# Performance work log

Hardware: AMD Instinct MI355X
Metric: run time of the kernel (lower is better)

Reference implementation:

```python
import jax, jax.numpy as jnp
import numpy as np

N_NODES = 100000
N_EDGES = 1600000
N_GRAPHS = 512


def gcn_conv(x, row, col, W, b):
    # x: [N, Cin], row/col: [E] (self-loops already appended)
    n = x.shape[0]
    h = x @ W                                        # [N, Cout]
    deg = jax.ops.segment_sum(jnp.ones_like(col, dtype=x.dtype), col, num_segments=n)
    dinv = jnp.where(deg > 0, deg ** -0.5, 0.0)
    norm = dinv[row] * dinv[col]                     # [E]
    msg = norm[:, None] * h[row]                     # [E, Cout]
    out = jax.ops.segment_sum(msg, col, num_segments=n)
    return out + b


def setup_inputs() -> dict:
    key = jax.random.key(0)
    ks = jax.random.split(key, 10)
    x = jax.random.normal(ks[0], (N_NODES, 128), dtype=jnp.float32)
    edge_index = jax.random.randint(ks[1], (2, N_EDGES), 0, N_NODES, dtype=jnp.int64)
    batch = jnp.sort(jax.random.randint(ks[2], (N_NODES,), 0, N_GRAPHS, dtype=jnp.int64))
    def lin_w(k, fan_in, fan_out):
        bound = 1.0 / np.sqrt(fan_in)
        return jax.random.uniform(k, (fan_in, fan_out), jnp.float32, -bound, bound)
    # GCN layers (bias zero-initialized per reset_parameters)
    W1 = lin_w(ks[3], 128, 128); b1 = jnp.zeros((128,), jnp.float32)
    W2 = lin_w(ks[4], 128, 128); b2 = jnp.zeros((128,), jnp.float32)
    # MLP layers (Linear with bias)
    Wm1 = lin_w(ks[5], 128, 64)
    bm1 = jax.random.uniform(ks[6], (64,), jnp.float32, -1/np.sqrt(128), 1/np.sqrt(128))
    Wm2 = lin_w(ks[7], 64, 1)
    bm2 = jax.random.uniform(ks[8], (1,), jnp.float32, -1/np.sqrt(64), 1/np.sqrt(64))
    return {"x": x, "edge_index": edge_index, "batch": batch,
            "W1": W1, "b1": b1, "W2": W2, "b2": b2,
            "Wm1": Wm1, "bm1": bm1, "Wm2": Wm2, "bm2": bm2}


def reference(x, edge_index, batch, W1, b1, W2, b2, Wm1, bm1, Wm2, bm2):
    n = x.shape[0]
    loops = jnp.arange(n, dtype=edge_index.dtype)
    row = jnp.concatenate([edge_index[0], loops])
    col = jnp.concatenate([edge_index[1], loops])
    # GCN: conv -> relu -> conv
    h = gcn_conv(x, row, col, W1, b1)
    h = jax.nn.relu(h)
    h = gcn_conv(h, row, col, W2, b2)
    # scatter-mean pooling over graphs
    sums = jax.ops.segment_sum(h, batch, num_segments=N_GRAPHS)      # [G, C]
    counts = jax.ops.segment_sum(jnp.ones((n,), h.dtype), batch, num_segments=N_GRAPHS)
    g = sums / jnp.maximum(counts, 1.0)[:, None]
    # MLP: linear -> relu -> linear
    g = jax.nn.relu(g @ Wm1 + bm1)
    out = g @ Wm2 + bm2
    return out
```

## Files before the change

kernel.cpp:

```cpp
#include <hip/hip_runtime.h>
#include <math.h>

#define C_DIM 128
#define POOL_CHUNK 64
#define BKT_SHIFT 7
#define MAX_B 1024
#define CB 256
typedef unsigned short ushort_t;
typedef __attribute__((ext_vector_type(8))) short short8;
typedef __attribute__((ext_vector_type(4))) float f32x4;

static inline int ceil_div(int a, int b) { return (a + b - 1) / b; }

__device__ inline ushort_t f2bf(float f) {
    union { float f; unsigned u; } v; v.f = f;
    unsigned r = v.u + 0x7FFFu + ((v.u >> 16) & 1u);
    return (ushort_t)(r >> 16);
}
__device__ inline float bf2f(unsigned s) {
    union { unsigned u; float f; } v; v.u = s << 16; return v.f;
}
__device__ inline float bf_lo(unsigned u) {
    union { unsigned v; float f; } c; c.v = u << 16; return c.f;
}
__device__ inline float bf_hi(unsigned u) {
    union { unsigned v; float f; } c; c.v = u & 0xFFFF0000u; return c.f;
}
__device__ inline void accum8(uint4 u, float acc[8]) {
    acc[0] += bf_lo(u.x); acc[1] += bf_hi(u.x);
    acc[2] += bf_lo(u.y); acc[3] += bf_hi(u.y);
    acc[4] += bf_lo(u.z); acc[5] += bf_hi(u.z);
    acc[6] += bf_lo(u.w); acc[7] += bf_hi(u.w);
}


__global__ __launch_bounds__(256) void k_bcount(
    const int* __restrict__ col, int E, int chunk, int B,
    int* __restrict__ counts) {
    __shared__ int hist[MAX_B];
    int t = threadIdx.x;
    for (int i = t; i < B; i += 256) hist[i] = 0;
    __syncthreads();
    int s = blockIdx.x * chunk;
    int e = s + chunk; if (e > E) e = E;
    for (int i = s + 4 * t; i < e; i += 1024) {
        int4 c = *(const int4*)(col + i);
        atomicAdd(&hist[c.x >> BKT_SHIFT], 1);
        atomicAdd(&hist[c.y >> BKT_SHIFT], 1);
        atomicAdd(&hist[c.z >> BKT_SHIFT], 1);
        atomicAdd(&hist[c.w >> BKT_SHIFT], 1);
    }
    __syncthreads();
    for (int i = t; i < B; i += 256)
        counts[(size_t)i * CB + blockIdx.x] = hist[i];
}

__global__ __launch_bounds__(256) void k_bscan(
    int* __restrict__ counts, int* __restrict__ btot) {
    __shared__ int sd[256];
    int b = blockIdx.x, t = threadIdx.x;
    int v = counts[(size_t)b * CB + t];
    sd[t] = v;
    __syncthreads();
    for (int off = 1; off < 256; off <<= 1) {
        int x = (t >= off) ? sd[t - off] : 0;
        __syncthreads();
        sd[t] += x;
        __syncthreads();
    }
    counts[(size_t)b * CB + t] = sd[t] - v;
    if (t == 255) btot[b] = sd[255];
}

__global__ __launch_bounds__(256) void k_btotscan(
    const int* __restrict__ btot, int* __restrict__ bbase, int B, int E,
    int* __restrict__ offs, int N) {
    __shared__ int sd[256];
    __shared__ int carry_s;
    int t = threadIdx.x;
    if (t == 0) carry_s = 0;
    __syncthreads();
    int nc = (B + 255) / 256;
    for (int c = 0; c < nc; ++c) {
        int idx = c * 256 + t;
        int v = (idx < B) ? btot[idx] : 0;
        sd[t] = v;
        __syncthreads();
        for (int off = 1; off < 256; off <<= 1) {
            int x = (t >= off) ? sd[t - off] : 0;
            __syncthreads();
            sd[t] += x;
            __syncthreads();
        }
        int pre = sd[t] - v + carry_s;
        if (idx < B) bbase[idx] = pre;
        __syncthreads();
        if (t == 0) carry_s += sd[255];
        __syncthreads();
    }
    if (t == 0) { bbase[B] = E; offs[N] = E; }
}

__global__ __launch_bounds__(256) void k_bscatter(
    const int* __restrict__ row, const int* __restrict__ col, int E, int chunk,
    int B, const int* __restrict__ counts, const int* __restrict__ bbase,
    int2* __restrict__ epk) {
    __shared__ int cur[MAX_B];
    int t = threadIdx.x, blk = blockIdx.x;
    for (int i = t; i < B; i += 256)
        cur[i] = bbase[i] + counts[(size_t)i * CB + blk];
    __syncthreads();
    int s = blk * chunk;
    int e = s + chunk; if (e > E) e = E;
    for (int i = s + 4 * t; i < e; i += 1024) {
        int4 c = *(const int4*)(col + i);
        int4 r = *(const int4*)(row + i);
        int s0 = atomicAdd(&cur[c.x >> BKT_SHIFT], 1); epk[s0] = make_int2(r.x, c.x);
        int s1 = atomicAdd(&cur[c.y >> BKT_SHIFT], 1); epk[s1] = make_int2(r.y, c.y);
        int s2 = atomicAdd(&cur[c.z >> BKT_SHIFT], 1); epk[s2] = make_int2(r.z, c.z);
        int s3 = atomicAdd(&cur[c.w >> BKT_SHIFT], 1); epk[s3] = make_int2(r.w, c.w);
    }
}

__global__ __launch_bounds__(256) void k_bfinal(
    const int2* __restrict__ epk, const int* __restrict__ bbase, int N,
    int* __restrict__ offs, float* __restrict__ dinv, int* __restrict__ csr) {
    __shared__ int cnt[128];
    __shared__ int pre[128];
    __shared__ int cur[128];
    int bkt = blockIdx.x, t = threadIdx.x;
    int s = bbase[bkt], e = bbase[bkt + 1];
    int base = bkt << BKT_SHIFT;
    int nn = N - base; if (nn > 128) nn = 128;
    if (t < 128) cnt[t] = 0;
    __syncthreads();
    for (int i = s + t; i < e; i += 256)
        atomicAdd(&cnt[epk[i].y & 127], 1);
    __syncthreads();
    if (t < 128) pre[t] = cnt[t];
    __syncthreads();
    for (int off = 1; off < 128; off <<= 1) {
        int x = (t >= off && t < 128) ? pre[t - off] : 0;
        __syncthreads();
        if (t < 128) pre[t] += x;
        __syncthreads();
    }
    if (t < 128) {
        int ex = pre[t] - cnt[t];
        cur[t] = ex;
        if (t < nn) {
            offs[base + t] = s + ex;
            dinv[base + t] = 1.0f / sqrtf((float)cnt[t] + 1.0f);
        }
    }
    __syncthreads();
    for (int i = s + t; i < e; i += 256) {
        int2 rc = epk[i];
        int slot = atomicAdd(&cur[rc.y & 127], 1);
        csr[s + slot] = rc.x;
    }
}

__global__ __launch_bounds__(256) void k_wfrag(
    const float* __restrict__ W, uint4* __restrict__ wf) {
    int t = threadIdx.x;
    for (int f = t; f < 2048; f += 256) {
        int lane = f & 63, kkn = f >> 6;
        int kk = kkn & 3, nt = kkn >> 2;
        int n = lane & 15, quad = lane >> 4;
        union { ushort_t h[8]; uint4 v; } u;
#pragma unroll
        for (int j = 0; j < 8; ++j)
            u.h[j] = f2bf(W[(size_t)(kk * 32 + quad * 8 + j) * C_DIM + nt * 16 + n]);
        wf[f] = u.v;
    }
}

template <int ABF16>
__global__ __launch_bounds__(256) void k_matmul_mfma(
    const float* __restrict__ Af, const ushort_t* __restrict__ Abf,
    const uint4* __restrict__ wfrag, const float* __restrict__ dinv,
    ushort_t* __restrict__ Cb, int N) {
    __shared__ __align__(16) ushort_t eb[64 * 136];
    int t = threadIdx.x;
    int wv = t >> 6, lane = t & 63;
    int n = lane & 15, quad = lane >> 4;
    int row0 = blockIdx.x * 64;
    int rowA = row0 + wv * 16 + n;
    int rowAc = rowA < N ? rowA : N - 1;

    f32x4 acc[8];
#pragma unroll
    for (int i = 0; i < 8; ++i) acc[i] = (f32x4){0.f, 0.f, 0.f, 0.f};

#pragma unroll
    for (int kk = 0; kk < 4; ++kk) {
        short8 a;
        if (ABF16) {
            uint4 u = *(const uint4*)(Abf + (size_t)rowAc * C_DIM + kk * 32 + quad * 8);
            union { uint4 v; short8 s; } c; c.v = u;
            a = c.s;
        } else {
            const float4* ap = (const float4*)(Af + (size_t)rowAc * C_DIM + kk * 32 + quad * 8);
            float4 f0 = ap[0], f1 = ap[1];
            union { ushort_t h[8]; short8 s; } c;
            c.h[0] = f2bf(f0.x); c.h[1] = f2bf(f0.y); c.h[2] = f2bf(f0.z); c.h[3] = f2bf(f0.w);
            c.h[4] = f2bf(f1.x); c.h[5] = f2bf(f1.y); c.h[6] = f2bf(f1.z); c.h[7] = f2bf(f1.w);
            a = c.s;
        }
#pragma unroll
        for (int nt = 0; nt < 8; ++nt) {
            uint4 bu = wfrag[(nt * 4 + kk) * 64 + lane];
            union { uint4 v; short8 s; } c; c.v = bu;
            acc[nt] = __builtin_amdgcn_mfma_f32_16x16x32_bf16(a, c.s, acc[nt], 0, 0, 0);
        }
    }

#pragma unroll
    for (int reg = 0; reg < 4; ++reg) {
        int rl = wv * 16 + quad * 4 + reg;
        int r = row0 + rl;
        float s = dinv[r < N ? r : N - 1];
#pragma unroll
        for (int nt = 0; nt < 8; ++nt)
            eb[rl * 136 + nt * 16 + n] = f2bf(acc[nt][reg] * s);
    }
    __syncthreads();
    int rows = N - row0; if (rows > 64) rows = 64;
    for (int idx = t; idx < 16 * 64; idx += 256) {
        int r = idx >> 4, c8 = idx & 15;
        if (r < rows)
            *(uint4*)(Cb + (size_t)(row0 + r) * C_DIM + c8 * 8) =
                *(const uint4*)&eb[r * 136 + c8 * 8];
    }
}

template <int RELU>
__global__ __launch_bounds__(256) void k_aggregate(
    const ushort_t* __restrict__ hs, const int* __restrict__ offs,
    const int* __restrict__ csr, const float* __restrict__ dinv,
    const float* __restrict__ bias, uint4* __restrict__ outV, int N) {
    int node = (blockIdx.x << 2) + (threadIdx.x >> 6);
    if (node >= N) return;
    int t = threadIdx.x & 63;
    int q = t >> 4;
    int fs = t & 15;
    int s = offs[node], e = offs[node + 1];

    float acc[8];
    {
        uint4 u = *(const uint4*)(hs + (size_t)node * C_DIM + fs * 8);
        float v[8];
        v[0] = bf_lo(u.x); v[1] = bf_hi(u.x);
        v[2] = bf_lo(u.y); v[3] = bf_hi(u.y);
        v[4] = bf_lo(u.z); v[5] = bf_hi(u.z);
        v[6] = bf_lo(u.w); v[7] = bf_hi(u.w);
#pragma unroll
        for (int i = 0; i < 8; ++i) acc[i] = (q == 0) ? v[i] : 0.f;
    }

    int j = s;
    for (; j + 16 <= e; j += 16) {
        int r[4];
#pragma unroll
        for (int b = 0; b < 4; ++b) r[b] = csr[j + b * 4 + q];
        uint4 u[4];
#pragma unroll
        for (int b = 0; b < 4; ++b)
            u[b] = *(const uint4*)(hs + (size_t)r[b] * C_DIM + fs * 8);
#pragma unroll
        for (int b = 0; b < 4; ++b) accum8(u[b], acc);
    }
    for (; j + 4 <= e; j += 4) {
        int r = csr[j + q];
        uint4 u = *(const uint4*)(hs + (size_t)r * C_DIM + fs * 8);
        accum8(u, acc);
    }
    if (j + q < e) {
        int r = csr[j + q];
        uint4 u = *(const uint4*)(hs + (size_t)r * C_DIM + fs * 8);
        accum8(u, acc);
    }

#pragma unroll
    for (int i = 0; i < 8; ++i) {
        acc[i] += __shfl_xor(acc[i], 16);
        acc[i] += __shfl_xor(acc[i], 32);
    }

    if (q == 0) {
        float dn = dinv[node];
        float4 b0 = *(const float4*)(bias + fs * 8);
        float4 b1 = *(const float4*)(bias + fs * 8 + 4);
        float o[8];
        o[0] = dn * acc[0] + b0.x; o[1] = dn * acc[1] + b0.y;
        o[2] = dn * acc[2] + b0.z; o[3] = dn * acc[3] + b0.w;
        o[4] = dn * acc[4] + b1.x; o[5] = dn * acc[5] + b1.y;
        o[6] = dn * acc[6] + b1.z; o[7] = dn * acc[7] + b1.w;
        if (RELU) {
#pragma unroll
            for (int i = 0; i < 8; ++i) o[i] = fmaxf(o[i], 0.f);
        }
        uint4 pk;
        pk.x = (unsigned)f2bf(o[0]) | ((unsigned)f2bf(o[1]) << 16);
        pk.y = (unsigned)f2bf(o[2]) | ((unsigned)f2bf(o[3]) << 16);
        pk.z = (unsigned)f2bf(o[4]) | ((unsigned)f2bf(o[5]) << 16);
        pk.w = (unsigned)f2bf(o[6]) | ((unsigned)f2bf(o[7]) << 16);
        outV[(size_t)node * 16 + fs] = pk;
    }
}

__global__ __launch_bounds__(128) void k_pool_sum(
    const ushort_t* __restrict__ h, const int* __restrict__ batch, int n,
    float* __restrict__ sums) {
    int r0 = blockIdx.x * POOL_CHUNK;
    int r1 = r0 + POOL_CHUNK; if (r1 > n) r1 = n;
    if (r0 >= n) return;
    int t = threadIdx.x;
    int g = batch[r0];
    float run = 0.f;
    int i = r0;
    while (i < r1) {
        if (i + 4 <= r1 && batch[i + 3] == g) {
            float a0 = bf2f(h[(size_t)i * C_DIM + t]);
            float a1 = bf2f(h[(size_t)(i + 1) * C_DIM + t]);
            float a2 = bf2f(h[(size_t)(i + 2) * C_DIM + t]);
            float a3 = bf2f(h[(size_t)(i + 3) * C_DIM + t]);
            run += (a0 + a1) + (a2 + a3);
            i += 4;
        } else {
            int bi = batch[i];
            if (bi != g) { atomicAdd(&sums[(size_t)g * C_DIM + t], run); run = 0.f; g = bi; }
            run += bf2f(h[(size_t)i * C_DIM + t]);
            ++i;
        }
    }
    atomicAdd(&sums[(size_t)g * C_DIM + t], run);
}

__global__ __launch_bounds__(128) void k_mlp(
    const float* __restrict__ sums, const int* __restrict__ batch, int n,
    const float* __restrict__ Wm1, const float* __restrict__ bm1,
    const float* __restrict__ Wm2, const float* __restrict__ bm2,
    float* __restrict__ out) {
    int g = blockIdx.x;
    int t = threadIdx.x;
    int lo = 0, hi = n;
    while (lo < hi) { int m = (lo + hi) >> 1; if (batch[m] < g) lo = m + 1; else hi = m; }
    int start = lo;
    lo = start; hi = n;
    while (lo < hi) { int m = (lo + hi) >> 1; if (batch[m] < g + 1) lo = m + 1; else hi = m; }
    float cnt = (float)(lo - start);

    float mean = sums[(size_t)g * C_DIM + t] / fmaxf(cnt, 1.0f);

    __shared__ float m_s[128];
    __shared__ float hid[64];
    m_s[t] = mean;
    __syncthreads();
    if (t < 64) {
        float a = bm1[t];
#pragma unroll 4
        for (int k = 0; k < 128; ++k) a += m_s[k] * Wm1[k * 64 + t];
        hid[t] = fmaxf(a, 0.f) * Wm2[t];
    }
    __syncthreads();
    if (t < 64) {
        float v = hid[t];
        for (int off = 32; off > 0; off >>= 1) v += __shfl_down(v, off);
        if (t == 0) out[g] = v + bm2[0];
    }
}

extern "C" void kernel_launch(void* const* d_in, const int* in_sizes, int n_in,
                              void* d_out, int out_size, void* d_ws, size_t ws_size,
                              hipStream_t stream) {
    const float* x     = (const float*)d_in[0];
    const int*   eidx  = (const int*)d_in[1];
    const int*   batch = (const int*)d_in[2];
    const float* W1    = (const float*)d_in[3];
    const float* b1    = (const float*)d_in[4];
    const float* W2    = (const float*)d_in[5];
    const float* b2    = (const float*)d_in[6];
    const float* Wm1   = (const float*)d_in[7];
    const float* bm1   = (const float*)d_in[8];
    const float* Wm2   = (const float*)d_in[9];
    const float* bm2   = (const float*)d_in[10];

    const int N = in_sizes[2];
    const int E = in_sizes[1] / 2;
    const int G = out_size;
    const int B = (N + 127) >> BKT_SHIFT;

    char* p = (char*)d_ws;
    auto carve = [&](size_t bytes) {
        char* q = p;
        p += (bytes + 255) & ~(size_t)255;
        return q;
    };
    ushort_t* bufT   = (ushort_t*)carve((size_t)N * C_DIM * sizeof(ushort_t));
    ushort_t* bufA   = (ushort_t*)carve((size_t)N * C_DIM * sizeof(ushort_t));
    float*    dinv   = (float*)   carve((size_t)N * sizeof(float));
    int*      offs   = (int*)     carve((size_t)(N + 1) * sizeof(int));
    int*      csr    = (int*)     carve((size_t)E * sizeof(int));
    int*      counts = (int*)     carve((size_t)B * CB * sizeof(int));
    int*      btot   = (int*)     carve((size_t)B * sizeof(int));
    int*      bbase  = (int*)     carve((size_t)(B + 1) * sizeof(int));
    float*    gsums  = (float*)   carve((size_t)G * C_DIM * sizeof(float));
    uint4*    wf1    = (uint4*)   carve(2048 * sizeof(uint4));
    uint4*    wf2    = (uint4*)   carve(2048 * sizeof(uint4));
    int2*     epk    = (int2*)bufT;

    const int* erow = eidx;
    const int* ecol = eidx + E;
    const int chunk = (ceil_div(E, CB) + 3) & ~3;

    hipMemsetAsync(gsums, 0, (size_t)G * C_DIM * sizeof(float), stream);

    k_bcount<<<CB, 256, 0, stream>>>(ecol, E, chunk, B, counts);
    k_bscan<<<B, 256, 0, stream>>>(counts, btot);
    k_btotscan<<<1, 256, 0, stream>>>(btot, bbase, B, E, offs, N);
    k_bscatter<<<CB, 256, 0, stream>>>(erow, ecol, E, chunk, B, counts, bbase, epk);
    k_bfinal<<<B, 256, 0, stream>>>(epk, bbase, N, offs, dinv, csr);

    k_wfrag<<<1, 256, 0, stream>>>(W1, wf1);
    k_wfrag<<<1, 256, 0, stream>>>(W2, wf2);

    k_matmul_mfma<0><<<ceil_div(N, 64), 256, 0, stream>>>(x, nullptr, wf1, dinv, bufT, N);
    k_aggregate<1><<<ceil_div(N, 4), 256, 0, stream>>>(bufT, offs, csr, dinv, b1,
                                                       (uint4*)bufA, N);
    k_matmul_mfma<1><<<ceil_div(N, 64), 256, 0, stream>>>(nullptr, bufA, wf2, dinv, bufT, N);
    k_aggregate<0><<<ceil_div(N, 4), 256, 0, stream>>>(bufT, offs, csr, dinv, b2,
                                                       (uint4*)bufA, N);
    k_pool_sum<<<ceil_div(N, POOL_CHUNK), 128, 0, stream>>>(bufA, batch, N, gsums);
    k_mlp<<<G, 128, 0, stream>>>(gsums, batch, N, Wm1, bm1, Wm2, bm2, (float*)d_out);
}
```

Baseline: 340.4 us.

## Pack edges into one int, stage buckets in LDS, widen matmul tiles, vectorize gathers

Edges in the bucket sort are packed as (row<<7 | col&127) in a single int, which halves the scatter traffic, and k_bfinal stages each bucket in shared memory so epk is read from global only once. The MFMA matmul now handles 128 rows per block and keeps the weight fragments in LDS. Two wfrag launches are merged into one. The aggregate kernel aligns its neighbor reads so it can load indices with int4, and the pool kernel reads two bf16 values per thread with two row groups. The costs are extra LDS use (32KB in bfinal, 32KB of weights in matmul), which may lower occupancy, and packing assumes row indices fit in 24 bits.

```diff
diff --git a/kernel.cpp b/kernel.cpp
--- a/kernel.cpp
+++ b/kernel.cpp
@@ -6,6 +6,7 @@
 #define BKT_SHIFT 7
 #define MAX_B 1024
 #define CB 256
+#define FB_CAP 8192
 typedef unsigned short ushort_t;
 typedef __attribute__((ext_vector_type(8))) short short8;
 typedef __attribute__((ext_vector_type(4))) float f32x4;
@@ -25,12 +26,6 @@
 }
 __device__ inline float bf_hi(unsigned u) {
     union { unsigned v; float f; } c; c.v = u & 0xFFFF0000u; return c.f;
-}
-__device__ inline void accum8(uint4 u, float acc[8]) {
-    acc[0] += bf_lo(u.x); acc[1] += bf_hi(u.x);
-    acc[2] += bf_lo(u.y); acc[3] += bf_hi(u.y);
-    acc[4] += bf_lo(u.z); acc[5] += bf_hi(u.z);
-    acc[6] += bf_lo(u.w); acc[7] += bf_hi(u.w);
 }
 
 
@@ -104,7 +99,7 @@
 __global__ __launch_bounds__(256) void k_bscatter(
     const int* __restrict__ row, const int* __restrict__ col, int E, int chunk,
     int B, const int* __restrict__ counts, const int* __restrict__ bbase,
-    int2* __restrict__ epk) {
+    int* __restrict__ epk) {
     __shared__ int cur[MAX_B];
     int t = threadIdx.x, blk = blockIdx.x;
     for (int i = t; i < B; i += 256)
@@ -115,27 +110,38 @@
     for (int i = s + 4 * t; i < e; i += 1024) {
         int4 c = *(const int4*)(col + i);
         int4 r = *(const int4*)(row + i);
-        int s0 = atomicAdd(&cur[c.x >> BKT_SHIFT], 1); epk[s0] = make_int2(r.x, c.x);
-        int s1 = atomicAdd(&cur[c.y >> BKT_SHIFT], 1); epk[s1] = make_int2(r.y, c.y);
-        int s2 = atomicAdd(&cur[c.z >> BKT_SHIFT], 1); epk[s2] = make_int2(r.z, c.z);
-        int s3 = atomicAdd(&cur[c.w >> BKT_SHIFT], 1); epk[s3] = make_int2(r.w, c.w);
+        int s0 = atomicAdd(&cur[c.x >> BKT_SHIFT], 1); epk[s0] = (r.x << 7) | (c.x & 127);
+        int s1 = atomicAdd(&cur[c.y >> BKT_SHIFT], 1); epk[s1] = (r.y << 7) | (c.y & 127);
+        int s2 = atomicAdd(&cur[c.z >> BKT_SHIFT], 1); epk[s2] = (r.z << 7) | (c.z & 127);
+        int s3 = atomicAdd(&cur[c.w >> BKT_SHIFT], 1); epk[s3] = (r.w << 7) | (c.w & 127);
     }
 }
 
 __global__ __launch_bounds__(256) void k_bfinal(
-    const int2* __restrict__ epk, const int* __restrict__ bbase, int N,
+    const int* __restrict__ epk, const int* __restrict__ bbase, int N,
     int* __restrict__ offs, float* __restrict__ dinv, int* __restrict__ csr) {
+    __shared__ int sh[FB_CAP];
     __shared__ int cnt[128];
     __shared__ int pre[128];
     __shared__ int cur[128];
     int bkt = blockIdx.x, t = threadIdx.x;
     int s = bbase[bkt], e = bbase[bkt + 1];
+    int m = e - s;
     int base = bkt << BKT_SHIFT;
     int nn = N - base; if (nn > 128) nn = 128;
+    bool fits = (m <= FB_CAP);
     if (t < 128) cnt[t] = 0;
     __syncthreads();
-    for (int i = s + t; i < e; i += 256)
-        atomicAdd(&cnt[epk[i].y & 127], 1);
+    if (fits) {
+        for (int i = t; i < m; i += 256) {
+            int u = epk[s + i];
+            sh[i] = u;
+            atomicAdd(&cnt[u & 127], 1);
+        }
+    } else {
+        for (int i = s + t; i < e; i += 256)
+            atomicAdd(&cnt[epk[i] & 127], 1);
+    }
     __syncthreads();
     if (t < 128) pre[t] = cnt[t];
     __syncthreads();
@@ -154,15 +160,26 @@
         }
     }
     __syncthreads();
-    for (int i = s + t; i < e; i += 256) {
-        int2 rc = epk[i];
-        int slot = atomicAdd(&cur[rc.y & 127], 1);
-        csr[s + slot] = rc.x;
-    }
-}
-
-__global__ __launch_bounds__(256) void k_wfrag(
-    const float* __restrict__ W, uint4* __restrict__ wf) {
+    if (fits) {
+        for (int i = t; i < m; i += 256) {
+            int u = sh[i];
+            int slot = atomicAdd(&cur[u & 127], 1);
+            csr[s + slot] = u >> 7;
+        }
+    } else {
+        for (int i = s + t; i < e; i += 256) {
+            int u = epk[i];
+            int slot = atomicAdd(&cur[u & 127], 1);
+            csr[s + slot] = u >> 7;
+        }
+    }
+}
+
+__global__ __launch_bounds__(256) void k_wfrag2(
+    const float* __restrict__ W1, const float* __restrict__ W2,
+    uint4* __restrict__ wf1, uint4* __restrict__ wf2) {
+    const float* W = blockIdx.x ? W2 : W1;
+    uint4* wf = blockIdx.x ? wf2 : wf1;
     int t = threadIdx.x;
     for (int f = t; f < 2048; f += 256) {
         int lane = f & 63, kkn = f >> 6;
@@ -181,57 +198,77 @@
     const float* __restrict__ Af, const ushort_t* __restrict__ Abf,
     const uint4* __restrict__ wfrag, const float* __restrict__ dinv,
     ushort_t* __restrict__ Cb, int N) {
+    __shared__ uint4 wfs[2048];
     __shared__ __align__(16) ushort_t eb[64 * 136];
     int t = threadIdx.x;
     int wv = t >> 6, lane = t & 63;
     int n = lane & 15, quad = lane >> 4;
-    int row0 = blockIdx.x * 64;
-    int rowA = row0 + wv * 16 + n;
-    int rowAc = rowA < N ? rowA : N - 1;
-
-    f32x4 acc[8];
-#pragma unroll
-    for (int i = 0; i < 8; ++i) acc[i] = (f32x4){0.f, 0.f, 0.f, 0.f};
+    int row0 = blockIdx.x * 128;
+
+    for (int i = t; i < 2048; i += 256) wfs[i] = wfrag[i];
+
+    int rA[2];
+#pragma unroll
+    for (int tl = 0; tl < 2; ++tl) {
+        int r = row0 + wv * 32 + tl * 16 + n;
+        rA[tl] = r < N ? r : N - 1;
+    }
+
+    f32x4 acc[2][8];
+#pragma unroll
+    for (int tl = 0; tl < 2; ++tl)
+#pragma unroll
+        for (int i = 0; i < 8; ++i) acc[tl][i] = (f32x4){0.f, 0.f, 0.f, 0.f};
+
+    __syncthreads();
 
 #pragma unroll
     for (int kk = 0; kk < 4; ++kk) {
-        short8 a;
-        if (ABF16) {
-            uint4 u = *(const uint4*)(Abf + (size_t)rowAc * C_DIM + kk * 32 + quad * 8);
-            union { uint4 v; short8 s; } c; c.v = u;
-            a = c.s;
-        } else {
-            const float4* ap = (const float4*)(Af + (size_t)rowAc * C_DIM + kk * 32 + quad * 8);
-            float4 f0 = ap[0], f1 = ap[1];
-            union { ushort_t h[8]; short8 s; } c;
-            c.h[0] = f2bf(f0.x); c.h[1] = f2bf(f0.y); c.h[2] = f2bf(f0.z); c.h[3] = f2bf(f0.w);
-            c.h[4] = f2bf(f1.x); c.h[5] = f2bf(f1.y); c.h[6] = f2bf(f1.z); c.h[7] = f2bf(f1.w);
-            a = c.s;
+        short8 a[2];
+#pragma unroll
+        for (int tl = 0; tl < 2; ++tl) {
+            if (ABF16) {
+                uint4 u = *(const uint4*)(Abf + (size_t)rA[tl] * C_DIM + kk * 32 + quad * 8);
+                union { uint4 v; short8 s; } c; c.v = u;
+                a[tl] = c.s;
+            } else {
+                const float4* ap = (const float4*)(Af + (size_t)rA[tl] * C_DIM + kk * 32 + quad * 8);
+                float4 f0 = ap[0], f1 = ap[1];
+                union { ushort_t h[8]; short8 s; } c;
+                c.h[0] = f2bf(f0.x); c.h[1] = f2bf(f0.y); c.h[2] = f2bf(f0.z); c.h[3] = f2bf(f0.w);
+                c.h[4] = f2bf(f1.x); c.h[5] = f2bf(f1.y); c.h[6] = f2bf(f1.z); c.h[7] = f2bf(f1.w);
+                a[tl] = c.s;
+            }
         }
 #pragma unroll
         for (int nt = 0; nt < 8; ++nt) {
-            uint4 bu = wfrag[(nt * 4 + kk) * 64 + lane];
+            uint4 bu = wfs[(nt * 4 + kk) * 64 + lane];
             union { uint4 v; short8 s; } c; c.v = bu;
-            acc[nt] = __builtin_amdgcn_mfma_f32_16x16x32_bf16(a, c.s, acc[nt], 0, 0, 0);
-        }
-    }
-
-#pragma unroll
-    for (int reg = 0; reg < 4; ++reg) {
-        int rl = wv * 16 + quad * 4 + reg;
-        int r = row0 + rl;
-        float s = dinv[r < N ? r : N - 1];
-#pragma unroll
-        for (int nt = 0; nt < 8; ++nt)
-            eb[rl * 136 + nt * 16 + n] = f2bf(acc[nt][reg] * s);
-    }
-    __syncthreads();
-    int rows = N - row0; if (rows > 64) rows = 64;
-    for (int idx = t; idx < 16 * 64; idx += 256) {
-        int r = idx >> 4, c8 = idx & 15;
-        if (r < rows)
-            *(uint4*)(Cb + (size_t)(row0 + r) * C_DIM + c8 * 8) =
-                *(const uint4*)&eb[r * 136 + c8 * 8];
+            acc[0][nt] = __builtin_amdgcn_mfma_f32_16x16x32_bf16(a[0], c.s, acc[0][nt], 0, 0, 0);
+            acc[1][nt] = __builtin_amdgcn_mfma_f32_16x16x32_bf16(a[1], c.s, acc[1][nt], 0, 0, 0);
+        }
+    }
+
+#pragma unroll
+    for (int pass = 0; pass < 2; ++pass) {
+        __syncthreads();
+#pragma unroll
+        for (int reg = 0; reg < 4; ++reg) {
+            int lr = quad * 4 + reg;
+            int grow = row0 + wv * 32 + pass * 16 + lr;
+            float sc = dinv[grow < N ? grow : N - 1];
+#pragma unroll
+            for (int nt = 0; nt < 8; ++nt)
+                eb[(wv * 16 + lr) * 136 + nt * 16 + n] = f2bf(acc[pass][nt][reg] * sc);
+        }
+        __syncthreads();
+        for (int idx = t; idx < 16 * 64; idx += 256) {
+            int r = idx >> 4, c8 = idx & 15;
+            int grow = row0 + (r >> 4) * 32 + pass * 16 + (r & 15);
+            if (grow < N)
+                *(uint4*)(Cb + (size_t)grow * C_DIM + c8 * 8) =
+                    *(const uint4*)&eb[r * 136 + c8 * 8];
+        }
     }
 }
 
@@ -247,45 +284,76 @@
     int fs = t & 15;
     int s = offs[node], e = offs[node + 1];
 
-    float acc[8];
+    float2 ac[4];
     {
         uint4 u = *(const uint4*)(hs + (size_t)node * C_DIM + fs * 8);
-        float v[8];
-        v[0] = bf_lo(u.x); v[1] = bf_hi(u.x);
-        v[2] = bf_lo(u.y); v[3] = bf_hi(u.y);
-        v[4] = bf_lo(u.z); v[5] = bf_hi(u.z);
-        v[6] = bf_lo(u.w); v[7] = bf_hi(u.w);
-#pragma unroll
-        for (int i = 0; i < 8; ++i) acc[i] = (q == 0) ? v[i] : 0.f;
+        if (q == 0) {
+            ac[0] = make_float2(bf_lo(u.x), bf_hi(u.x));
+            ac[1] = make_float2(bf_lo(u.y), bf_hi(u.y));
+            ac[2] = make_float2(bf_lo(u.z), bf_hi(u.z));
+            ac[3] = make_float2(bf_lo(u.w), bf_hi(u.w));
+        } else {
+#pragma unroll
+            for (int i = 0; i < 4; ++i) ac[i] = make_float2(0.f, 0.f);
+        }
     }
 
     int j = s;
+    int head = (s + 3) & ~3; if (head > e) head = e;
+    if (j < head) {
+        if (j + q < head) {
+            uint4 u = *(const uint4*)(hs + (size_t)csr[j + q] * C_DIM + fs * 8);
+            ac[0].x += bf_lo(u.x); ac[0].y += bf_hi(u.x);
+            ac[1].x += bf_lo(u.y); ac[1].y += bf_hi(u.y);
+            ac[2].x += bf_lo(u.z); ac[2].y += bf_hi(u.z);
+            ac[3].x += bf_lo(u.w); ac[3].y += bf_hi(u.w);
+        }
+        j = head;
+    }
     for (; j + 16 <= e; j += 16) {
-        int r[4];
-#pragma unroll
-        for (int b = 0; b < 4; ++b) r[b] = csr[j + b * 4 + q];
-        uint4 u[4];
-#pragma unroll
-        for (int b = 0; b < 4; ++b)
-            u[b] = *(const uint4*)(hs + (size_t)r[b] * C_DIM + fs * 8);
-#pragma unroll
-        for (int b = 0; b < 4; ++b) accum8(u[b], acc);
+        int4 rv = *(const int4*)(csr + j + 4 * q);
+        uint4 u0 = *(const uint4*)(hs + (size_t)rv.x * C_DIM + fs * 8);
+        uint4 u1 = *(const uint4*)(hs + (size_t)rv.y * C_DIM + fs * 8);
+        uint4 u2 = *(const uint4*)(hs + (size_t)rv.z * C_DIM + fs * 8);
+        uint4 u3 = *(const uint4*)(hs + (size_t)rv.w * C_DIM + fs * 8);
+        ac[0].x += bf_lo(u0.x); ac[0].y += bf_hi(u0.x);
+        ac[1].x += bf_lo(u0.y); ac[1].y += bf_hi(u0.y);
+        ac[2].x += bf_lo(u0.z); ac[2].y += bf_hi(u0.z);
+        ac[3].x += bf_lo(u0.w); ac[3].y += bf_hi(u0.w);
+        ac[0].x += bf_lo(u1.x); ac[0].y += bf_hi(u1.x);
+        ac[1].x += bf_lo(u1.y); ac[1].y += bf_hi(u1.y);
+        ac[2].x += bf_lo(u1.z); ac[2].y += bf_hi(u1.z);
+        ac[3].x += bf_lo(u1.w); ac[3].y += bf_hi(u1.w);
+        ac[0].x += bf_lo(u2.x); ac[0].y += bf_hi(u2.x);
+        ac[1].x += bf_lo(u2.y); ac[1].y += bf_hi(u2.y);
+        ac[2].x += bf_lo(u2.z); ac[2].y += bf_hi(u2.z);
+        ac[3].x += bf_lo(u2.w); ac[3].y += bf_hi(u2.w);
+        ac[0].x += bf_lo(u3.x); ac[0].y += bf_hi(u3.x);
+        ac[1].x += bf_lo(u3.y); ac[1].y += bf_hi(u3.y);
+        ac[2].x += bf_lo(u3.z); ac[2].y += bf_hi(u3.z);
+        ac[3].x += bf_lo(u3.w); ac[3].y += bf_hi(u3.w);
     }
     for (; j + 4 <= e; j += 4) {
-        int r = csr[j + q];
-        uint4 u = *(const uint4*)(hs + (size_t)r * C_DIM + fs * 8);
-        accum8(u, acc);
+        uint4 u = *(const uint4*)(hs + (size_t)csr[j + q] * C_DIM + fs * 8);
+        ac[0].x += bf_lo(u.x); ac[0].y += bf_hi(u.x);
+        ac[1].x += bf_lo(u.y); ac[1].y += bf_hi(u.y);
+        ac[2].x += bf_lo(u.z); ac[2].y += bf_hi(u.z);
+        ac[3].x += bf_lo(u.w); ac[3].y += bf_hi(u.w);
     }
     if (j + q < e) {
-        int r = csr[j + q];
-        uint4 u = *(const uint4*)(hs + (size_t)r * C_DIM + fs * 8);
-        accum8(u, acc);
-    }
-
-#pragma unroll
-    for (int i = 0; i < 8; ++i) {
-        acc[i] += __shfl_xor(acc[i], 16);
-        acc[i] += __shfl_xor(acc[i], 32);
+        uint4 u = *(const uint4*)(hs + (size_t)csr[j + q] * C_DIM + fs * 8);
+        ac[0].x += bf_lo(u.x); ac[0].y += bf_hi(u.x);
+        ac[1].x += bf_lo(u.y); ac[1].y += bf_hi(u.y);
+        ac[2].x += bf_lo(u.z); ac[2].y += bf_hi(u.z);
+        ac[3].x += bf_lo(u.w); ac[3].y += bf_hi(u.w);
+    }
+
+#pragma unroll
+    for (int i = 0; i < 4; ++i) {
+        ac[i].x += __shfl_xor(ac[i].x, 16);
+        ac[i].y += __shfl_xor(ac[i].y, 16);
+        ac[i].x += __shfl_xor(ac[i].x, 32);
+        ac[i].y += __shfl_xor(ac[i].y, 32);
     }
 
     if (q == 0) {
@@ -293,10 +361,10 @@
         float4 b0 = *(const float4*)(bias + fs * 8);
         float4 b1 = *(const float4*)(bias + fs * 8 + 4);
         float o[8];
-        o[0] = dn * acc[0] + b0.x; o[1] = dn * acc[1] + b0.y;
-        o[2] = dn * acc[2] + b0.z; o[3] = dn * acc[3] + b0.w;
-        o[4] = dn * acc[4] + b1.x; o[5] = dn * acc[5] + b1.y;
-        o[6] = dn * acc[6] + b1.z; o[7] = dn * acc[7] + b1.w;
+        o[0] = dn * ac[0].x + b0.x; o[1] = dn * ac[0].y + b0.y;
+        o[2] = dn * ac[1].x + b0.z; o[3] = dn * ac[1].y + b0.w;
+        o[4] = dn * ac[2].x + b1.x; o[5] = dn * ac[2].y + b1.y;
+        o[6] = dn * ac[3].x + b1.z; o[7] = dn * ac[3].y + b1.w;
         if (RELU) {
 #pragma unroll
             for (int i = 0; i < 8; ++i) o[i] = fmaxf(o[i], 0.f);
@@ -317,25 +385,34 @@
     int r1 = r0 + POOL_CHUNK; if (r1 > n) r1 = n;
     if (r0 >= n) return;
     int t = threadIdx.x;
+    int c = t & 63, rr = t >> 6;
+    float2 acc = make_float2(0.f, 0.f);
     int g = batch[r0];
-    float run = 0.f;
     int i = r0;
     while (i < r1) {
-        if (i + 4 <= r1 && batch[i + 3] == g) {
-            float a0 = bf2f(h[(size_t)i * C_DIM + t]);
-            float a1 = bf2f(h[(size_t)(i + 1) * C_DIM + t]);
-            float a2 = bf2f(h[(size_t)(i + 2) * C_DIM + t]);
-            float a3 = bf2f(h[(size_t)(i + 3) * C_DIM + t]);
-            run += (a0 + a1) + (a2 + a3);
-            i += 4;
+        if (i + 8 <= r1 && batch[i + 7] == g) {
+#pragma unroll
+            for (int b = 0; b < 4; ++b) {
+                unsigned u = *(const unsigned*)(h + (size_t)(i + rr + 2 * b) * C_DIM + c * 2);
+                acc.x += bf_lo(u); acc.y += bf_hi(u);
+            }
+            i += 8;
         } else {
             int bi = batch[i];
-            if (bi != g) { atomicAdd(&sums[(size_t)g * C_DIM + t], run); run = 0.f; g = bi; }
-            run += bf2f(h[(size_t)i * C_DIM + t]);
+            if (bi != g) {
+                atomicAdd(&sums[(size_t)g * C_DIM + c * 2], acc.x);
+                atomicAdd(&sums[(size_t)g * C_DIM + c * 2 + 1], acc.y);
+                acc = make_float2(0.f, 0.f); g = bi;
+            }
+            if (rr == 0) {
+                unsigned u = *(const unsigned*)(h + (size_t)i * C_DIM + c * 2);
+                acc.x += bf_lo(u); acc.y += bf_hi(u);
+            }
             ++i;
         }
     }
-    atomicAdd(&sums[(size_t)g * C_DIM + t], run);
+    atomicAdd(&sums[(size_t)g * C_DIM + c * 2], acc.x);
+    atomicAdd(&sums[(size_t)g * C_DIM + c * 2 + 1], acc.y);
 }
 
 __global__ __launch_bounds__(128) void k_mlp(
@@ -409,7 +486,7 @@
     float*    gsums  = (float*)   carve((size_t)G * C_DIM * sizeof(float));
     uint4*    wf1    = (uint4*)   carve(2048 * sizeof(uint4));
     uint4*    wf2    = (uint4*)   carve(2048 * sizeof(uint4));
-    int2*     epk    = (int2*)bufT;
+    int*      epk    = (int*)bufT;
 
     const int* erow = eidx;
     const int* ecol = eidx + E;
@@ -423,13 +500,12 @@
     k_bscatter<<<CB, 256, 0, stream>>>(erow, ecol, E, chunk, B, counts, bbase, epk);
     k_bfinal<<<B, 256, 0, stream>>>(epk, bbase, N, offs, dinv, csr);
 
-    k_wfrag<<<1, 256, 0, stream>>>(W1, wf1);
-    k_wfrag<<<1, 256, 0, stream>>>(W2, wf2);
-
-    k_matmul_mfma<0><<<ceil_div(N, 64), 256, 0, stream>>>(x, nullptr, wf1, dinv, bufT, N);
+    k_wfrag2<<<2, 256, 0, stream>>>(W1, W2, wf1, wf2);
+
+    k_matmul_mfma<0><<<ceil_div(N, 128), 256, 0, stream>>>(x, nullptr, wf1, dinv, bufT, N);
     k_aggregate<1><<<ceil_div(N, 4), 256, 0, stream>>>(bufT, offs, csr, dinv, b1,
                                                        (uint4*)bufA, N);
-    k_matmul_mfma<1><<<ceil_div(N, 64), 256, 0, stream>>>(nullptr, bufA, wf2, dinv, bufT, N);
+    k_matmul_mfma<1><<<ceil_div(N, 128), 256, 0, stream>>>(nullptr, bufA, wf2, dinv, bufT, N);
     k_aggregate<0><<<ceil_div(N, 4), 256, 0, stream>>>(bufT, offs, csr, dinv, b2,
                                                        (uint4*)bufA, N);
     k_pool_sum<<<ceil_div(N, POOL_CHUNK), 128, 0, stream>>>(bufA, batch, N, gsums);
```

New measurement: 341.7 us. No clear change (+0.4%).
